# Performance work log

Hardware: AMD Instinct MI355X
Metric: run time of the kernel (lower is better)

## Reference

```python
import jax, jax.numpy as jnp
import numpy as np

B, L, D, H = 2, 4096, 512, 8
DK = D // H
SCALE = 1.0 / float(np.sqrt(DK))


def setup_inputs() -> dict:
    key = jax.random.key(0)
    k1, k2, k3 = jax.random.split(key, 3)
    x = jax.random.normal(k1, (B, L, D), dtype=jnp.float32)
    w_qkv = jax.random.normal(k2, (3 * D, D), dtype=jnp.float32) * 0.02
    w_o = jax.random.normal(k3, (D, D), dtype=jnp.float32) * 0.02
    return {"x": x, "w_qkv": w_qkv, "w_o": w_o}


def reference(x, w_qkv, w_o):
    b, l, d = x.shape
    # qkv projection: Linear(d, 3d, bias=False) -> x @ W^T
    qkv = (x @ w_qkv.T).reshape(b, l, 3, H, DK).transpose(2, 0, 3, 1, 4)  # [3,B,H,L,dk]
    q, k, v = qkv[0], qkv[1], qkv[2]
    # naive O(L^2) attention (faithful to source)
    scores = jnp.einsum("bhld,bhmd->bhlm", q, k) * SCALE  # [B,H,L,L]
    attn = jax.nn.softmax(scores, axis=-1)
    ctx = jnp.einsum("bhlm,bhmd->bhld", attn, v)  # [B,H,L,dk]
    ctx = ctx.transpose(0, 2, 1, 3).reshape(b, l, d)
    return ctx @ w_o.T
```

## Files before the change

### kernel.cpp

```cpp
#include <hip/hip_runtime.h>


#define Bq 2
#define Lq 4096
#define Dq 512
#define Hq 8
#define DKq 64
#define PST 72

using short8  = __attribute__((ext_vector_type(8))) short;
using float4v = __attribute__((ext_vector_type(4))) float;
using half4   = __attribute__((ext_vector_type(4))) _Float16;
typedef unsigned short u16;
typedef unsigned int   u32;

__device__ __forceinline__ u16 f2bf(float f) {
    u32 u = __float_as_uint(f);
    u += 0x7fffu + ((u >> 16) & 1u);
    return (u16)(u >> 16);
}

__device__ __forceinline__ float4v mfma16(short8 a, short8 b, float4v c) {
    return __builtin_amdgcn_mfma_f32_16x16x32_bf16(a, b, c, 0, 0, 0);
}

__device__ __forceinline__ void gload_lds16(const u16* g, u16* l) {
    __builtin_amdgcn_global_load_lds(
        (const __attribute__((address_space(1))) unsigned int*)g,
        (__attribute__((address_space(3))) unsigned int*)l,
        16, 0, 0);
}

__global__ __launch_bounds__(256) void castall(const float* __restrict__ x,
                                               const float* __restrict__ wq,
                                               const float* __restrict__ wo,
                                               u16* __restrict__ xb,
                                               u16* __restrict__ wqb,
                                               u16* __restrict__ wob) {
    int g = blockIdx.x;
    const float* s; u16* d; int base;
    if (g < 4096)      { s = x;  d = xb;  base = g * 1024; }
    else if (g < 4864) { s = wq; d = wqb; base = (g - 4096) * 1024; }
    else               { s = wo; d = wob; base = (g - 4864) * 1024; }
    int i = base + threadIdx.x * 4;
    float4 f = *(const float4*)&s[i];
    ushort4 o;
    o.x = f2bf(f.x); o.y = f2bf(f.y); o.z = f2bf(f.z); o.w = f2bf(f.w);
    *(ushort4*)&d[i] = o;
}

__global__ __launch_bounds__(256) void qkv_gemm(const u16* __restrict__ A,
                                                const u16* __restrict__ Bw,
                                                u16* __restrict__ qb,
                                                u16* __restrict__ kb,
                                                u16* __restrict__ vt) {
    __shared__ __align__(16) u16 As[128 * 64];
    __shared__ __align__(16) u16 Bs[128 * 64];
    const int m0 = blockIdx.x * 128, n0 = blockIdx.y * 128;
    const int tid = threadIdx.x, w = tid >> 6, lane = tid & 63;
    const int l15 = lane & 15, quad = lane >> 4;
    const int wy = w & 1, wx = w >> 1;
    const int r8 = lane >> 3, c8 = lane & 7, csw = c8 ^ r8;
    const int sw = l15 & 7;

    float4v acc[4][4];
    float4v zero = {0.f, 0.f, 0.f, 0.f};
#pragma unroll
    for (int mi = 0; mi < 4; mi++)
#pragma unroll
        for (int ni = 0; ni < 4; ni++) acc[mi][ni] = zero;

    for (int k0 = 0; k0 < 512; k0 += 64) {
#pragma unroll
        for (int i = 0; i < 4; i++) {
            int row = w * 32 + i * 8;
            gload_lds16(&A[(size_t)(m0 + row + r8) * 512 + k0 + csw * 8], &As[row * 64]);
            gload_lds16(&Bw[(size_t)(n0 + row + r8) * 512 + k0 + csw * 8], &Bs[row * 64]);
        }
        __syncthreads();
        short8 af0[4], af1[4], bf0[4], bf1[4];
#pragma unroll
        for (int t = 0; t < 4; t++) {
            int rowA = wy * 64 + t * 16 + l15;
            af0[t] = *(const short8*)&As[rowA * 64 + ((quad ^ sw) * 8)];
            af1[t] = *(const short8*)&As[rowA * 64 + (((quad + 4) ^ sw) * 8)];
            int rowB = wx * 64 + t * 16 + l15;
            bf0[t] = *(const short8*)&Bs[rowB * 64 + ((quad ^ sw) * 8)];
            bf1[t] = *(const short8*)&Bs[rowB * 64 + (((quad + 4) ^ sw) * 8)];
        }
#pragma unroll
        for (int mi = 0; mi < 4; mi++)
#pragma unroll
            for (int ni = 0; ni < 4; ni++) {
                acc[mi][ni] = mfma16(af0[mi], bf0[ni], acc[mi][ni]);
                acc[mi][ni] = mfma16(af1[mi], bf1[ni], acc[mi][ni]);
            }
        __syncthreads();
    }

#pragma unroll
    for (int mi = 0; mi < 4; mi++)
#pragma unroll
        for (int ni = 0; ni < 4; ni++) {
            int i0 = m0 + wy * 64 + mi * 16 + quad * 4;
            int j  = n0 + wx * 64 + ni * 16 + l15;
            int sel = j >> 9, rem = j & 511, h = rem >> 6, dk = rem & 63;
            int b = i0 >> 12, l = i0 & 4095;
            if (sel == 2) {
                ushort4 v4;
                v4.x = f2bf(acc[mi][ni][0]); v4.y = f2bf(acc[mi][ni][1]);
                v4.z = f2bf(acc[mi][ni][2]); v4.w = f2bf(acc[mi][ni][3]);
                *(ushort4*)&vt[((size_t)(b * Hq + h) * DKq + dk) * Lq + l] = v4;
            } else {
                u16* tgt = (sel == 0) ? qb : kb;
                float sc = (sel == 0) ? 0.125f : 1.0f;
#pragma unroll
                for (int r = 0; r < 4; r++)
                    tgt[((size_t)(b * Hq + h) * Lq + (l + r)) * DKq + dk] = f2bf(acc[mi][ni][r] * sc);
            }
        }
}

__global__ __launch_bounds__(256, 4) void attn_kern(const u16* __restrict__ qb,
                                                    const u16* __restrict__ kb,
                                                    const u16* __restrict__ vt,
                                                    _Float16* __restrict__ op0,
                                                    _Float16* __restrict__ op1,
                                                    float* __restrict__ denp) {
    __shared__ __align__(16) u16 Ks[64 * 64];
    __shared__ __align__(16) u16 Vs[64 * 64];
    __shared__ __align__(16) u16 Ps[4 * 32 * PST];
    const int g = blockIdx.x;
    const int xcd = g & 7, idx = g >> 3;
    const int bh = xcd * 2 + (idx & 1);
    const int rest = idx >> 1;
    const int split = rest & 1;
    const int q0 = (rest >> 1) * 128;
    const int tid = threadIdx.x;
    const int w = tid >> 6, lane = tid & 63, l15 = lane & 15, quad = lane >> 4;
    const int r8 = lane >> 3, c8 = lane & 7, csw = c8 ^ r8;
    const int sw = l15 & 7;

    const u16* qbase = qb + (size_t)bh * Lq * DKq;
    const u16* kbase = kb + (size_t)bh * Lq * DKq;
    const u16* vbase = vt + (size_t)bh * DKq * Lq;

    short8 aq0[2], aq1[2];
#pragma unroll
    for (int s = 0; s < 2; s++) {
        int qrow = q0 + w * 32 + s * 16 + l15;
        aq0[s] = *(const short8*)&qbase[(size_t)qrow * DKq + quad * 8];
        aq1[s] = *(const short8*)&qbase[(size_t)qrow * DKq + 32 + quad * 8];
    }

    short8 ones;
#pragma unroll
    for (int j = 0; j < 8; j++) ones[j] = (short)0x3F80;

    float4v zero = {0.f, 0.f, 0.f, 0.f};
    float4v oacc[2][4], den[2];
#pragma unroll
    for (int s = 0; s < 2; s++) {
        den[s] = zero;
#pragma unroll
        for (int n = 0; n < 4; n++) oacc[s][n] = zero;
    }

    u16* Pw = Ps + w * 32 * PST;
    const int j0base = split * 2048;

    for (int jt = 0; jt < 32; jt++) {
        int j0 = j0base + jt * 64;
        if (w < 2) {
#pragma unroll
            for (int i = 0; i < 4; i++) {
                int base = w * 32 + i * 8;
                gload_lds16(&kbase[(size_t)(j0 + base + r8) * DKq + csw * 8], &Ks[base * 64]);
            }
        } else {
#pragma unroll
            for (int i = 0; i < 4; i++) {
                int base = (w - 2) * 32 + i * 8;
                gload_lds16(&vbase[(size_t)(base + r8) * Lq + j0 + csw * 8], &Vs[base * 64]);
            }
        }
        __syncthreads();

        short8 kf0[4], kf1[4], vf0[4], vf1[4];
#pragma unroll
        for (int n = 0; n < 4; n++) {
            int row = n * 16 + l15;
            kf0[n] = *(const short8*)&Ks[row * 64 + ((quad ^ sw) * 8)];
            kf1[n] = *(const short8*)&Ks[row * 64 + (((quad + 4) ^ sw) * 8)];
            vf0[n] = *(const short8*)&Vs[row * 64 + ((quad ^ sw) * 8)];
            vf1[n] = *(const short8*)&Vs[row * 64 + (((quad + 4) ^ sw) * 8)];
        }

#pragma unroll
        for (int s = 0; s < 2; s++) {
#pragma unroll
            for (int nk = 0; nk < 4; nk++) {
                float4v sv = zero;
                sv = mfma16(kf0[nk], aq0[s], sv);
                sv = mfma16(kf1[nk], aq1[s], sv);
                u32 u0 = __float_as_uint(__expf(sv[0])) + 0x8000u;
                u32 u1 = __float_as_uint(__expf(sv[1])) + 0x8000u;
                u32 u2 = __float_as_uint(__expf(sv[2])) + 0x8000u;
                u32 u3 = __float_as_uint(__expf(sv[3])) + 0x8000u;
                uint2 pv;
                pv.x = __builtin_amdgcn_perm(u1, u0, 0x07060302u);
                pv.y = __builtin_amdgcn_perm(u3, u2, 0x07060302u);
                *(uint2*)&Pw[(s * 16 + l15) * PST + nk * 16 + quad * 4] = pv;
            }
        }

#pragma unroll
        for (int s = 0; s < 2; s++) {
            short8 ap0 = *(const short8*)&Pw[(s * 16 + l15) * PST + quad * 8];
            short8 ap1 = *(const short8*)&Pw[(s * 16 + l15) * PST + 32 + quad * 8];
            den[s] = mfma16(ap0, ones, den[s]);
            den[s] = mfma16(ap1, ones, den[s]);
#pragma unroll
            for (int n = 0; n < 4; n++) {
                oacc[s][n] = mfma16(ap0, vf0[n], oacc[s][n]);
                oacc[s][n] = mfma16(ap1, vf1[n], oacc[s][n]);
            }
        }
        __syncthreads();
    }

    _Float16* op = split ? op1 : op0;
#pragma unroll
    for (int s = 0; s < 2; s++)
#pragma unroll
        for (int r = 0; r < 4; r++) {
            float dv = den[s][r];
            float rd = __builtin_amdgcn_rcpf(dv);
            int row = q0 + w * 32 + s * 16 + quad * 4 + r;
            if (l15 == 0) denp[(size_t)(split * 16 + bh) * Lq + row] = dv;
#pragma unroll
            for (int n = 0; n < 4; n++)
                op[((size_t)bh * Lq + row) * DKq + n * 16 + l15] =
                    (_Float16)(oacc[s][n][r] * rd);
        }
}

__global__ __launch_bounds__(256) void combine(const _Float16* __restrict__ op0,
                                               const _Float16* __restrict__ op1,
                                               const float* __restrict__ denp,
                                               u16* __restrict__ ctxq) {
    int t = blockIdx.x * 256 + threadIdx.x;
    int dk4 = t & 15, l = (t >> 4) & 4095, bh = t >> 16;
    size_t r0 = (size_t)bh * Lq + l;
    half4 h0 = *(const half4*)&op0[r0 * DKq + dk4 * 4];
    half4 h1 = *(const half4*)&op1[r0 * DKq + dk4 * 4];
    float d0 = denp[r0];
    float d1 = denp[(size_t)(16 + bh) * Lq + l];
    float rs = __builtin_amdgcn_rcpf(d0 + d1);
    int b = bh >> 3, h = bh & 7;
    ushort4 o;
    o.x = f2bf(((float)h0.x * d0 + (float)h1.x * d1) * rs);
    o.y = f2bf(((float)h0.y * d0 + (float)h1.y * d1) * rs);
    o.z = f2bf(((float)h0.z * d0 + (float)h1.z * d1) * rs);
    o.w = f2bf(((float)h0.w * d0 + (float)h1.w * d1) * rs);
    *(ushort4*)&ctxq[((size_t)(b * Lq + l)) * Dq + h * DKq + dk4 * 4] = o;
}

__global__ __launch_bounds__(256) void out_gemm(const u16* __restrict__ A,
                                                const u16* __restrict__ Bw,
                                                float* __restrict__ out) {
    __shared__ __align__(16) u16 As[128 * 64];
    __shared__ __align__(16) u16 Bs[128 * 64];
    const int m0 = blockIdx.x * 128, n0 = blockIdx.y * 128;
    const int tid = threadIdx.x, w = tid >> 6, lane = tid & 63;
    const int l15 = lane & 15, quad = lane >> 4;
    const int wy = w & 1, wx = w >> 1;
    const int r8 = lane >> 3, c8 = lane & 7, csw = c8 ^ r8;
    const int sw = l15 & 7;

    float4v acc[4][4];
    float4v zero = {0.f, 0.f, 0.f, 0.f};
#pragma unroll
    for (int mi = 0; mi < 4; mi++)
#pragma unroll
        for (int ni = 0; ni < 4; ni++) acc[mi][ni] = zero;

    for (int k0 = 0; k0 < 512; k0 += 64) {
#pragma unroll
        for (int i = 0; i < 4; i++) {
            int row = w * 32 + i * 8;
            gload_lds16(&A[(size_t)(m0 + row + r8) * 512 + k0 + csw * 8], &As[row * 64]);
            gload_lds16(&Bw[(size_t)(n0 + row + r8) * 512 + k0 + csw * 8], &Bs[row * 64]);
        }
        __syncthreads();
        short8 af0[4], af1[4], bf0[4], bf1[4];
#pragma unroll
        for (int t = 0; t < 4; t++) {
            int rowA = wy * 64 + t * 16 + l15;
            af0[t] = *(const short8*)&As[rowA * 64 + ((quad ^ sw) * 8)];
            af1[t] = *(const short8*)&As[rowA * 64 + (((quad + 4) ^ sw) * 8)];
            int rowB = wx * 64 + t * 16 + l15;
            bf0[t] = *(const short8*)&Bs[rowB * 64 + ((quad ^ sw) * 8)];
            bf1[t] = *(const short8*)&Bs[rowB * 64 + (((quad + 4) ^ sw) * 8)];
        }
#pragma unroll
        for (int mi = 0; mi < 4; mi++)
#pragma unroll
            for (int ni = 0; ni < 4; ni++) {
                acc[mi][ni] = mfma16(af0[mi], bf0[ni], acc[mi][ni]);
                acc[mi][ni] = mfma16(af1[mi], bf1[ni], acc[mi][ni]);
            }
        __syncthreads();
    }

#pragma unroll
    for (int mi = 0; mi < 4; mi++)
#pragma unroll
        for (int ni = 0; ni < 4; ni++)
#pragma unroll
            for (int r = 0; r < 4; r++) {
                int i = m0 + wy * 64 + mi * 16 + quad * 4 + r;
                int j = n0 + wx * 64 + ni * 16 + l15;
                out[(size_t)i * 512 + j] = acc[mi][ni][r];
            }
}

extern "C" void kernel_launch(void* const* d_in, const int* in_sizes, int n_in,
                              void* d_out, int out_size, void* d_ws, size_t ws_size,
                              hipStream_t stream) {
    const float* x     = (const float*)d_in[0];
    const float* w_qkv = (const float*)d_in[1];
    const float* w_o   = (const float*)d_in[2];
    float* out = (float*)d_out;

    const size_t N_X   = (size_t)Bq * Lq * Dq;
    const size_t N_WQ  = (size_t)3 * Dq * Dq;
    const size_t N_WO  = (size_t)Dq * Dq;
    const size_t N_QKV = (size_t)Bq * Hq * Lq * DKq;

    u16* xb  = (u16*)d_ws;
    u16* wqb = xb + N_X;
    u16* wob = wqb + N_WQ;
    u16* qb  = wob + N_WO;
    u16* kb  = qb + N_QKV;
    u16* vt  = kb + N_QKV;
    u16* o1r = vt + N_QKV;

    _Float16* op0  = (_Float16*)xb;
    _Float16* op1  = (_Float16*)o1r;
    float*    denp = (float*)wqb;
    u16*      ctxq = qb;

    castall<<<dim3(5120), 256, 0, stream>>>(x, w_qkv, w_o, xb, wqb, wob);
    qkv_gemm<<<dim3(64, 12), 256, 0, stream>>>(xb, wqb, qb, kb, vt);
    attn_kern<<<dim3(1024), 256, 0, stream>>>(qb, kb, vt, op0, op1, denp);
    combine<<<dim3(4096), 256, 0, stream>>>(op0, op1, denp, ctxq);
    out_gemm<<<dim3(64, 4), 256, 0, stream>>>(ctxq, wob, out);
}
```

Baseline: 198.9 us.

## Rework attention tiling with double-buffered K/V and LDS-staged GEMM epilogues

The attention kernel now gives each wave a 64-query by 32-key quadrant instead of 32 queries by all 64 keys. It keeps P in registers and feeds it straight into 16x16x16 bf16 MFMAs, which removes the LDS round trip for P. K/V tiles are double-buffered so the next tile loads while the current one is computed, and partial sums from the two key-halves are reduced through LDS at the end. Separately, the QKV and output GEMM epilogues stage results in padded LDS so global stores are wide and coalesced (including the V transpose). The costs are more registers per wave (the occupancy hint was dropped), extra synchronisation for the cross-wave reduction, and use of the smaller MFMA shape.

```diff
diff --git a/kernel.cpp b/kernel.cpp
--- a/kernel.cpp
+++ b/kernel.cpp
@@ -6,9 +6,10 @@
 #define Dq 512
 #define Hq 8
 #define DKq 64
-#define PST 72
 
 using short8  = __attribute__((ext_vector_type(8))) short;
+using short4v = __attribute__((ext_vector_type(4))) short;
+using ushort8 = __attribute__((ext_vector_type(8))) unsigned short;
 using float4v = __attribute__((ext_vector_type(4))) float;
 using half4   = __attribute__((ext_vector_type(4))) _Float16;
 typedef unsigned short u16;
@@ -22,6 +23,17 @@
 
 __device__ __forceinline__ float4v mfma16(short8 a, short8 b, float4v c) {
     return __builtin_amdgcn_mfma_f32_16x16x32_bf16(a, b, c, 0, 0, 0);
+}
+
+__device__ __forceinline__ float4v mfma1k(short4v a, short4v b, float4v c) {
+#if __has_builtin(__builtin_amdgcn_mfma_f32_16x16x16bf16_1k)
+    return __builtin_amdgcn_mfma_f32_16x16x16bf16_1k(a, b, c, 0, 0, 0);
+#else
+    float4v d;
+    asm volatile("v_mfma_f32_16x16x16_bf16 %0, %1, %2, %3"
+                 : "=v"(d) : "v"(a), "v"(b), "v"(c));
+    return d;
+#endif
 }
 
 __device__ __forceinline__ void gload_lds16(const u16* g, u16* l) {
@@ -54,8 +66,10 @@
                                                 u16* __restrict__ qb,
                                                 u16* __restrict__ kb,
                                                 u16* __restrict__ vt) {
-    __shared__ __align__(16) u16 As[128 * 64];
-    __shared__ __align__(16) u16 Bs[128 * 64];
+    __shared__ __align__(16) union {
+        struct { u16 A[128 * 64]; u16 B[128 * 64]; } s;
+        u16 epi[128 * 134];
+    } sm;
     const int m0 = blockIdx.x * 128, n0 = blockIdx.y * 128;
     const int tid = threadIdx.x, w = tid >> 6, lane = tid & 63;
     const int l15 = lane & 15, quad = lane >> 4;
@@ -74,19 +88,19 @@
 #pragma unroll
         for (int i = 0; i < 4; i++) {
             int row = w * 32 + i * 8;
-            gload_lds16(&A[(size_t)(m0 + row + r8) * 512 + k0 + csw * 8], &As[row * 64]);
-            gload_lds16(&Bw[(size_t)(n0 + row + r8) * 512 + k0 + csw * 8], &Bs[row * 64]);
+            gload_lds16(&A[(size_t)(m0 + row + r8) * 512 + k0 + csw * 8], &sm.s.A[row * 64]);
+            gload_lds16(&Bw[(size_t)(n0 + row + r8) * 512 + k0 + csw * 8], &sm.s.B[row * 64]);
         }
         __syncthreads();
         short8 af0[4], af1[4], bf0[4], bf1[4];
 #pragma unroll
         for (int t = 0; t < 4; t++) {
             int rowA = wy * 64 + t * 16 + l15;
-            af0[t] = *(const short8*)&As[rowA * 64 + ((quad ^ sw) * 8)];
-            af1[t] = *(const short8*)&As[rowA * 64 + (((quad + 4) ^ sw) * 8)];
+            af0[t] = *(const short8*)&sm.s.A[rowA * 64 + ((quad ^ sw) * 8)];
+            af1[t] = *(const short8*)&sm.s.A[rowA * 64 + (((quad + 4) ^ sw) * 8)];
             int rowB = wx * 64 + t * 16 + l15;
-            bf0[t] = *(const short8*)&Bs[rowB * 64 + ((quad ^ sw) * 8)];
-            bf1[t] = *(const short8*)&Bs[rowB * 64 + (((quad + 4) ^ sw) * 8)];
+            bf0[t] = *(const short8*)&sm.s.B[rowB * 64 + ((quad ^ sw) * 8)];
+            bf1[t] = *(const short8*)&sm.s.B[rowB * 64 + (((quad + 4) ^ sw) * 8)];
         }
 #pragma unroll
         for (int mi = 0; mi < 4; mi++)
@@ -98,46 +112,66 @@
         __syncthreads();
     }
 
-#pragma unroll
-    for (int mi = 0; mi < 4; mi++)
-#pragma unroll
-        for (int ni = 0; ni < 4; ni++) {
-            int i0 = m0 + wy * 64 + mi * 16 + quad * 4;
-            int j  = n0 + wx * 64 + ni * 16 + l15;
-            int sel = j >> 9, rem = j & 511, h = rem >> 6, dk = rem & 63;
-            int b = i0 >> 12, l = i0 & 4095;
-            if (sel == 2) {
+    const int sel = n0 >> 9;
+    if (sel < 2) {
+        const float sc = (sel == 0) ? 0.125f : 1.0f;
+#pragma unroll
+        for (int mi = 0; mi < 4; mi++)
+#pragma unroll
+            for (int ni = 0; ni < 4; ni++)
+#pragma unroll
+                for (int r = 0; r < 4; r++)
+                    sm.epi[(wy * 64 + mi * 16 + quad * 4 + r) * 134 + wx * 64 + ni * 16 + l15] =
+                        f2bf(acc[mi][ni][r] * sc);
+        __syncthreads();
+        u16* tgt = (sel == 0) ? qb : kb;
+#pragma unroll
+        for (int i = 0; i < 8; i++) {
+            int flat = i * 2048 + tid * 8;
+            int row = flat >> 7, col = flat & 127;
+            ushort8 vv = *(const ushort8*)&sm.epi[row * 134 + col];
+            int dg = (n0 & 511) + col, h = dg >> 6, dk = dg & 63;
+            int mm = m0 + row, b = mm >> 12, l = mm & 4095;
+            *(ushort8*)&tgt[((size_t)(b * Hq + h) * Lq + l) * DKq + dk] = vv;
+        }
+    } else {
+#pragma unroll
+        for (int mi = 0; mi < 4; mi++)
+#pragma unroll
+            for (int ni = 0; ni < 4; ni++) {
                 ushort4 v4;
                 v4.x = f2bf(acc[mi][ni][0]); v4.y = f2bf(acc[mi][ni][1]);
                 v4.z = f2bf(acc[mi][ni][2]); v4.w = f2bf(acc[mi][ni][3]);
-                *(ushort4*)&vt[((size_t)(b * Hq + h) * DKq + dk) * Lq + l] = v4;
-            } else {
-                u16* tgt = (sel == 0) ? qb : kb;
-                float sc = (sel == 0) ? 0.125f : 1.0f;
-#pragma unroll
-                for (int r = 0; r < 4; r++)
-                    tgt[((size_t)(b * Hq + h) * Lq + (l + r)) * DKq + dk] = f2bf(acc[mi][ni][r] * sc);
-            }
-        }
-}
-
-__global__ __launch_bounds__(256, 4) void attn_kern(const u16* __restrict__ qb,
-                                                    const u16* __restrict__ kb,
-                                                    const u16* __restrict__ vt,
-                                                    _Float16* __restrict__ op0,
-                                                    _Float16* __restrict__ op1,
-                                                    float* __restrict__ denp) {
-    __shared__ __align__(16) u16 Ks[64 * 64];
-    __shared__ __align__(16) u16 Vs[64 * 64];
-    __shared__ __align__(16) u16 Ps[4 * 32 * PST];
+                *(ushort4*)&sm.epi[(wx * 64 + ni * 16 + l15) * 134 + wy * 64 + mi * 16 + quad * 4] = v4;
+            }
+        __syncthreads();
+#pragma unroll
+        for (int i = 0; i < 8; i++) {
+            int flat = i * 2048 + tid * 8;
+            int vrow = flat >> 7, vcol = flat & 127;
+            ushort8 vv = *(const ushort8*)&sm.epi[vrow * 134 + vcol];
+            int dg = (n0 & 511) + vrow, h = dg >> 6, dk = dg & 63;
+            int mm = m0 + vcol, b = mm >> 12, l = mm & 4095;
+            *(ushort8*)&vt[((size_t)(b * Hq + h) * DKq + dk) * Lq + l] = vv;
+        }
+    }
+}
+
+__global__ __launch_bounds__(256) void attn_kern(const u16* __restrict__ qb,
+                                                 const u16* __restrict__ kb,
+                                                 const u16* __restrict__ vt,
+                                                 _Float16* __restrict__ op0,
+                                                 _Float16* __restrict__ op1,
+                                                 float* __restrict__ denp) {
+    __shared__ __align__(16) u16 KV[2][2][64 * 64];
     const int g = blockIdx.x;
-    const int xcd = g & 7, idx = g >> 3;
-    const int bh = xcd * 2 + (idx & 1);
-    const int rest = idx >> 1;
+    const int bh = (g & 7) * 2 + ((g >> 3) & 1);
+    const int rest = g >> 4;
     const int split = rest & 1;
     const int q0 = (rest >> 1) * 128;
     const int tid = threadIdx.x;
     const int w = tid >> 6, lane = tid & 63, l15 = lane & 15, quad = lane >> 4;
+    const int wq = w & 1, wk = w >> 1;
     const int r8 = lane >> 3, c8 = lane & 7, csw = c8 ^ r8;
     const int sw = l15 & 7;
 
@@ -145,104 +179,146 @@
     const u16* kbase = kb + (size_t)bh * Lq * DKq;
     const u16* vbase = vt + (size_t)bh * DKq * Lq;
 
-    short8 aq0[2], aq1[2];
-#pragma unroll
-    for (int s = 0; s < 2; s++) {
-        int qrow = q0 + w * 32 + s * 16 + l15;
+    short8 aq0[4], aq1[4];
+#pragma unroll
+    for (int s = 0; s < 4; s++) {
+        int qrow = q0 + wq * 64 + s * 16 + l15;
         aq0[s] = *(const short8*)&qbase[(size_t)qrow * DKq + quad * 8];
         aq1[s] = *(const short8*)&qbase[(size_t)qrow * DKq + 32 + quad * 8];
     }
 
-    short8 ones;
-#pragma unroll
-    for (int j = 0; j < 8; j++) ones[j] = (short)0x3F80;
-
+    short4v ones4 = {(short)0x3F80, (short)0x3F80, (short)0x3F80, (short)0x3F80};
     float4v zero = {0.f, 0.f, 0.f, 0.f};
-    float4v oacc[2][4], den[2];
-#pragma unroll
-    for (int s = 0; s < 2; s++) {
+    float4v oacc[4][4], den[4];
+#pragma unroll
+    for (int s = 0; s < 4; s++) {
         den[s] = zero;
 #pragma unroll
         for (int n = 0; n < 4; n++) oacc[s][n] = zero;
     }
 
-    u16* Pw = Ps + w * 32 * PST;
     const int j0base = split * 2048;
-
-    for (int jt = 0; jt < 32; jt++) {
-        int j0 = j0base + jt * 64;
+    {
+        int j0 = j0base;
         if (w < 2) {
 #pragma unroll
             for (int i = 0; i < 4; i++) {
                 int base = w * 32 + i * 8;
-                gload_lds16(&kbase[(size_t)(j0 + base + r8) * DKq + csw * 8], &Ks[base * 64]);
+                gload_lds16(&kbase[(size_t)(j0 + base + r8) * DKq + csw * 8], &KV[0][0][base * 64]);
             }
         } else {
 #pragma unroll
             for (int i = 0; i < 4; i++) {
                 int base = (w - 2) * 32 + i * 8;
-                gload_lds16(&vbase[(size_t)(base + r8) * Lq + j0 + csw * 8], &Vs[base * 64]);
-            }
-        }
-        __syncthreads();
-
-        short8 kf0[4], kf1[4], vf0[4], vf1[4];
-#pragma unroll
-        for (int n = 0; n < 4; n++) {
-            int row = n * 16 + l15;
-            kf0[n] = *(const short8*)&Ks[row * 64 + ((quad ^ sw) * 8)];
-            kf1[n] = *(const short8*)&Ks[row * 64 + (((quad + 4) ^ sw) * 8)];
-            vf0[n] = *(const short8*)&Vs[row * 64 + ((quad ^ sw) * 8)];
-            vf1[n] = *(const short8*)&Vs[row * 64 + (((quad + 4) ^ sw) * 8)];
-        }
-
-#pragma unroll
-        for (int s = 0; s < 2; s++) {
-#pragma unroll
-            for (int nk = 0; nk < 4; nk++) {
-                float4v sv = zero;
-                sv = mfma16(kf0[nk], aq0[s], sv);
-                sv = mfma16(kf1[nk], aq1[s], sv);
+                gload_lds16(&vbase[(size_t)(base + r8) * Lq + j0 + csw * 8], &KV[0][1][base * 64]);
+            }
+        }
+    }
+
+    int p = 0;
+    for (int jt = 0; jt < 32; jt++) {
+        __syncthreads();
+        if (jt < 31) {
+            int j0 = j0base + (jt + 1) * 64;
+            if (w < 2) {
+#pragma unroll
+                for (int i = 0; i < 4; i++) {
+                    int base = w * 32 + i * 8;
+                    gload_lds16(&kbase[(size_t)(j0 + base + r8) * DKq + csw * 8], &KV[p ^ 1][0][base * 64]);
+                }
+            } else {
+#pragma unroll
+                for (int i = 0; i < 4; i++) {
+                    int base = (w - 2) * 32 + i * 8;
+                    gload_lds16(&vbase[(size_t)(base + r8) * Lq + j0 + csw * 8], &KV[p ^ 1][1][base * 64]);
+                }
+            }
+        }
+        const u16* Kb = KV[p][0];
+        const u16* Vb = KV[p][1];
+#pragma unroll
+        for (int nkk = 0; nkk < 2; nkk++) {
+            int krow = wk * 32 + nkk * 16 + l15;
+            short8 k0 = *(const short8*)&Kb[krow * 64 + ((quad ^ sw) * 8)];
+            short8 k1 = *(const short8*)&Kb[krow * 64 + (((quad + 4) ^ sw) * 8)];
+            int kc = ((wk * 4 + nkk * 2 + (quad >> 1)) ^ sw) * 8 + (quad & 1) * 4;
+            short4v vf[4];
+#pragma unroll
+            for (int n = 0; n < 4; n++)
+                vf[n] = *(const short4v*)&Vb[(n * 16 + l15) * 64 + kc];
+#pragma unroll
+            for (int s = 0; s < 4; s++) {
+                float4v sv = mfma16(k0, aq0[s], zero);
+                sv = mfma16(k1, aq1[s], sv);
                 u32 u0 = __float_as_uint(__expf(sv[0])) + 0x8000u;
                 u32 u1 = __float_as_uint(__expf(sv[1])) + 0x8000u;
                 u32 u2 = __float_as_uint(__expf(sv[2])) + 0x8000u;
                 u32 u3 = __float_as_uint(__expf(sv[3])) + 0x8000u;
-                uint2 pv;
-                pv.x = __builtin_amdgcn_perm(u1, u0, 0x07060302u);
-                pv.y = __builtin_amdgcn_perm(u3, u2, 0x07060302u);
-                *(uint2*)&Pw[(s * 16 + l15) * PST + nk * 16 + quad * 4] = pv;
-            }
-        }
-
-#pragma unroll
-        for (int s = 0; s < 2; s++) {
-            short8 ap0 = *(const short8*)&Pw[(s * 16 + l15) * PST + quad * 8];
-            short8 ap1 = *(const short8*)&Pw[(s * 16 + l15) * PST + 32 + quad * 8];
-            den[s] = mfma16(ap0, ones, den[s]);
-            den[s] = mfma16(ap1, ones, den[s]);
-#pragma unroll
-            for (int n = 0; n < 4; n++) {
-                oacc[s][n] = mfma16(ap0, vf0[n], oacc[s][n]);
-                oacc[s][n] = mfma16(ap1, vf1[n], oacc[s][n]);
-            }
-        }
-        __syncthreads();
-    }
-
-    _Float16* op = split ? op1 : op0;
-#pragma unroll
-    for (int s = 0; s < 2; s++)
-#pragma unroll
-        for (int r = 0; r < 4; r++) {
-            float dv = den[s][r];
-            float rd = __builtin_amdgcn_rcpf(dv);
-            int row = q0 + w * 32 + s * 16 + quad * 4 + r;
-            if (l15 == 0) denp[(size_t)(split * 16 + bh) * Lq + row] = dv;
-#pragma unroll
-            for (int n = 0; n < 4; n++)
-                op[((size_t)bh * Lq + row) * DKq + n * 16 + l15] =
-                    (_Float16)(oacc[s][n][r] * rd);
-        }
+                union { uint2 u; short4v s4; } cv;
+                cv.u.x = __builtin_amdgcn_perm(u1, u0, 0x07060302u);
+                cv.u.y = __builtin_amdgcn_perm(u3, u2, 0x07060302u);
+                short4v pf = cv.s4;
+                den[s] = mfma1k(pf, ones4, den[s]);
+#pragma unroll
+                for (int n = 0; n < 4; n++)
+                    oacc[s][n] = mfma1k(pf, vf[n], oacc[s][n]);
+            }
+        }
+        p ^= 1;
+    }
+    __syncthreads();
+
+    float4v* sc4 = (float4v*)&KV[0][0][0];
+    if (wk == 1) {
+        float4v* dst = sc4 + (size_t)(wq * 64 + lane) * 13;
+#pragma unroll
+        for (int s = 0; s < 4; s++) dst[s] = den[s];
+#pragma unroll
+        for (int s = 0; s < 2; s++)
+#pragma unroll
+            for (int n = 0; n < 4; n++) dst[4 + s * 4 + n] = oacc[s][n];
+    }
+    __syncthreads();
+    if (wk == 0) {
+        float4v* src = sc4 + (size_t)(wq * 64 + lane) * 13;
+#pragma unroll
+        for (int s = 0; s < 4; s++) den[s] += src[s];
+#pragma unroll
+        for (int s = 0; s < 2; s++)
+#pragma unroll
+            for (int n = 0; n < 4; n++) oacc[s][n] += src[4 + s * 4 + n];
+    }
+    __syncthreads();
+    if (wk == 1) {
+        float4v* dst = sc4 + (size_t)(wq * 64 + lane) * 9;
+#pragma unroll
+        for (int s = 2; s < 4; s++)
+#pragma unroll
+            for (int n = 0; n < 4; n++) dst[(s - 2) * 4 + n] = oacc[s][n];
+    }
+    __syncthreads();
+    if (wk == 0) {
+        float4v* src = sc4 + (size_t)(wq * 64 + lane) * 9;
+#pragma unroll
+        for (int s = 2; s < 4; s++)
+#pragma unroll
+            for (int n = 0; n < 4; n++) oacc[s][n] += src[(s - 2) * 4 + n];
+
+        _Float16* op = split ? op1 : op0;
+#pragma unroll
+        for (int s = 0; s < 4; s++)
+#pragma unroll
+            for (int r = 0; r < 4; r++) {
+                float dv = den[s][r];
+                float rd = __builtin_amdgcn_rcpf(dv);
+                int row = q0 + wq * 64 + s * 16 + quad * 4 + r;
+                if (l15 == 0) denp[(size_t)(split * 16 + bh) * Lq + row] = dv;
+#pragma unroll
+                for (int n = 0; n < 4; n++)
+                    op[((size_t)bh * Lq + row) * DKq + n * 16 + l15] =
+                        (_Float16)(oacc[s][n][r] * rd);
+            }
+    }
 }
 
 __global__ __launch_bounds__(256) void combine(const _Float16* __restrict__ op0,
@@ -269,8 +345,10 @@
 __global__ __launch_bounds__(256) void out_gemm(const u16* __restrict__ A,
                                                 const u16* __restrict__ Bw,
                                                 float* __restrict__ out) {
-    __shared__ __align__(16) u16 As[128 * 64];
-    __shared__ __align__(16) u16 Bs[128 * 64];
+    __shared__ __align__(16) union {
+        struct { u16 A[128 * 64]; u16 B[128 * 64]; } s;
+        float fepi[64 * 132];
+    } sm;
     const int m0 = blockIdx.x * 128, n0 = blockIdx.y * 128;
     const int tid = threadIdx.x, w = tid >> 6, lane = tid & 63;
     const int l15 = lane & 15, quad = lane >> 4;
@@ -289,19 +367,19 @@
 #pragma unroll
         for (int i = 0; i < 4; i++) {
             int row = w * 32 + i * 8;
-            gload_lds16(&A[(size_t)(m0 + row + r8) * 512 + k0 + csw * 8], &As[row * 64]);
-            gload_lds16(&Bw[(size_t)(n0 + row + r8) * 512 + k0 + csw * 8], &Bs[row * 64]);
+            gload_lds16(&A[(size_t)(m0 + row + r8) * 512 + k0 + csw * 8], &sm.s.A[row * 64]);
+            gload_lds16(&Bw[(size_t)(n0 + row + r8) * 512 + k0 + csw * 8], &sm.s.B[row * 64]);
         }
         __syncthreads();
         short8 af0[4], af1[4], bf0[4], bf1[4];
 #pragma unroll
         for (int t = 0; t < 4; t++) {
             int rowA = wy * 64 + t * 16 + l15;
-            af0[t] = *(const short8*)&As[rowA * 64 + ((quad ^ sw) * 8)];
-            af1[t] = *(const short8*)&As[rowA * 64 + (((quad + 4) ^ sw) * 8)];
+            af0[t] = *(const short8*)&sm.s.A[rowA * 64 + ((quad ^ sw) * 8)];
+            af1[t] = *(const short8*)&sm.s.A[rowA * 64 + (((quad + 4) ^ sw) * 8)];
             int rowB = wx * 64 + t * 16 + l15;
-            bf0[t] = *(const short8*)&Bs[rowB * 64 + ((quad ^ sw) * 8)];
-            bf1[t] = *(const short8*)&Bs[rowB * 64 + (((quad + 4) ^ sw) * 8)];
+            bf0[t] = *(const short8*)&sm.s.B[rowB * 64 + ((quad ^ sw) * 8)];
+            bf1[t] = *(const short8*)&sm.s.B[rowB * 64 + (((quad + 4) ^ sw) * 8)];
         }
 #pragma unroll
         for (int mi = 0; mi < 4; mi++)
@@ -314,15 +392,28 @@
     }
 
 #pragma unroll
-    for (int mi = 0; mi < 4; mi++)
-#pragma unroll
-        for (int ni = 0; ni < 4; ni++)
-#pragma unroll
-            for (int r = 0; r < 4; r++) {
-                int i = m0 + wy * 64 + mi * 16 + quad * 4 + r;
-                int j = n0 + wx * 64 + ni * 16 + l15;
-                out[(size_t)i * 512 + j] = acc[mi][ni][r];
-            }
+    for (int ph = 0; ph < 2; ph++) {
+#pragma unroll
+        for (int mh = 0; mh < 2; mh++) {
+            int mi = ph * 2 + mh;
+            int lr = wy * 32 + mh * 16 + quad * 4;
+#pragma unroll
+            for (int ni = 0; ni < 4; ni++)
+#pragma unroll
+                for (int r = 0; r < 4; r++)
+                    sm.fepi[(lr + r) * 132 + wx * 64 + ni * 16 + l15] = acc[mi][ni][r];
+        }
+        __syncthreads();
+#pragma unroll
+        for (int i = 0; i < 8; i++) {
+            int flat = i * 1024 + tid * 4;
+            int lrow = flat >> 7, col = flat & 127;
+            float4 vv = *(const float4*)&sm.fepi[lrow * 132 + col];
+            int m = (lrow & 31) + (lrow >> 5) * 64 + ph * 32;
+            *(float4*)&out[(size_t)(m0 + m) * 512 + n0 + col] = vv;
+        }
+        __syncthreads();
+    }
 }
 
 extern "C" void kernel_launch(void* const* d_in, const int* in_sizes, int n_in,
```

Measured after the change: 207.3 us. +4.2%, slower.

## Fuse split-combine into output GEMM and stage GEMM epilogues through LDS

Applied to the files above, without the earlier changes.

Drops the separate combine kernel. The output GEMM now reads the two fp16 partial attention outputs and their denominators, normalises them, and writes bf16 tiles straight into shared memory. The QKV and output GEMM epilogues now stage results in LDS and write coalesced 16-byte vectors instead of scattered scalar stores. The attention P buffer swaps row padding for an XOR swizzle. This removes one launch and an intermediate round trip through memory. In exchange the output GEMM repeats the combine math for each of its 4 column blocks and loses the async load path for A.

```diff
diff --git a/kernel.cpp b/kernel.cpp
--- a/kernel.cpp
+++ b/kernel.cpp
@@ -6,11 +6,10 @@
 #define Dq 512
 #define Hq 8
 #define DKq 64
-#define PST 72
 
 using short8  = __attribute__((ext_vector_type(8))) short;
+using ushort8 = __attribute__((ext_vector_type(8))) unsigned short;
 using float4v = __attribute__((ext_vector_type(4))) float;
-using half4   = __attribute__((ext_vector_type(4))) _Float16;
 typedef unsigned short u16;
 typedef unsigned int   u32;
 
@@ -54,8 +53,10 @@
                                                 u16* __restrict__ qb,
                                                 u16* __restrict__ kb,
                                                 u16* __restrict__ vt) {
-    __shared__ __align__(16) u16 As[128 * 64];
-    __shared__ __align__(16) u16 Bs[128 * 64];
+    __shared__ __align__(16) union {
+        struct { u16 A[128 * 64]; u16 B[128 * 64]; } s;
+        u16 epi[128 * 134];
+    } sm;
     const int m0 = blockIdx.x * 128, n0 = blockIdx.y * 128;
     const int tid = threadIdx.x, w = tid >> 6, lane = tid & 63;
     const int l15 = lane & 15, quad = lane >> 4;
@@ -74,19 +75,19 @@
 #pragma unroll
         for (int i = 0; i < 4; i++) {
             int row = w * 32 + i * 8;
-            gload_lds16(&A[(size_t)(m0 + row + r8) * 512 + k0 + csw * 8], &As[row * 64]);
-            gload_lds16(&Bw[(size_t)(n0 + row + r8) * 512 + k0 + csw * 8], &Bs[row * 64]);
+            gload_lds16(&A[(size_t)(m0 + row + r8) * 512 + k0 + csw * 8], &sm.s.A[row * 64]);
+            gload_lds16(&Bw[(size_t)(n0 + row + r8) * 512 + k0 + csw * 8], &sm.s.B[row * 64]);
         }
         __syncthreads();
         short8 af0[4], af1[4], bf0[4], bf1[4];
 #pragma unroll
         for (int t = 0; t < 4; t++) {
             int rowA = wy * 64 + t * 16 + l15;
-            af0[t] = *(const short8*)&As[rowA * 64 + ((quad ^ sw) * 8)];
-            af1[t] = *(const short8*)&As[rowA * 64 + (((quad + 4) ^ sw) * 8)];
+            af0[t] = *(const short8*)&sm.s.A[rowA * 64 + ((quad ^ sw) * 8)];
+            af1[t] = *(const short8*)&sm.s.A[rowA * 64 + (((quad + 4) ^ sw) * 8)];
             int rowB = wx * 64 + t * 16 + l15;
-            bf0[t] = *(const short8*)&Bs[rowB * 64 + ((quad ^ sw) * 8)];
-            bf1[t] = *(const short8*)&Bs[rowB * 64 + (((quad + 4) ^ sw) * 8)];
+            bf0[t] = *(const short8*)&sm.s.B[rowB * 64 + ((quad ^ sw) * 8)];
+            bf1[t] = *(const short8*)&sm.s.B[rowB * 64 + (((quad + 4) ^ sw) * 8)];
         }
 #pragma unroll
         for (int mi = 0; mi < 4; mi++)
@@ -98,27 +99,49 @@
         __syncthreads();
     }
 
-#pragma unroll
-    for (int mi = 0; mi < 4; mi++)
-#pragma unroll
-        for (int ni = 0; ni < 4; ni++) {
-            int i0 = m0 + wy * 64 + mi * 16 + quad * 4;
-            int j  = n0 + wx * 64 + ni * 16 + l15;
-            int sel = j >> 9, rem = j & 511, h = rem >> 6, dk = rem & 63;
-            int b = i0 >> 12, l = i0 & 4095;
-            if (sel == 2) {
+    const int sel = n0 >> 9;
+    if (sel < 2) {
+        const float sc = (sel == 0) ? 0.125f : 1.0f;
+#pragma unroll
+        for (int mi = 0; mi < 4; mi++)
+#pragma unroll
+            for (int ni = 0; ni < 4; ni++)
+#pragma unroll
+                for (int r = 0; r < 4; r++)
+                    sm.epi[(wy * 64 + mi * 16 + quad * 4 + r) * 134 + wx * 64 + ni * 16 + l15] =
+                        f2bf(acc[mi][ni][r] * sc);
+        __syncthreads();
+        u16* tgt = (sel == 0) ? qb : kb;
+#pragma unroll
+        for (int i = 0; i < 8; i++) {
+            int flat = i * 2048 + tid * 8;
+            int row = flat >> 7, col = flat & 127;
+            ushort8 vv = *(const ushort8*)&sm.epi[row * 134 + col];
+            int dg = (n0 & 511) + col, h = dg >> 6, dk = dg & 63;
+            int mm = m0 + row, b = mm >> 12, l = mm & 4095;
+            *(ushort8*)&tgt[((size_t)(b * Hq + h) * Lq + l) * DKq + dk] = vv;
+        }
+    } else {
+#pragma unroll
+        for (int mi = 0; mi < 4; mi++)
+#pragma unroll
+            for (int ni = 0; ni < 4; ni++) {
                 ushort4 v4;
                 v4.x = f2bf(acc[mi][ni][0]); v4.y = f2bf(acc[mi][ni][1]);
                 v4.z = f2bf(acc[mi][ni][2]); v4.w = f2bf(acc[mi][ni][3]);
-                *(ushort4*)&vt[((size_t)(b * Hq + h) * DKq + dk) * Lq + l] = v4;
-            } else {
-                u16* tgt = (sel == 0) ? qb : kb;
-                float sc = (sel == 0) ? 0.125f : 1.0f;
-#pragma unroll
-                for (int r = 0; r < 4; r++)
-                    tgt[((size_t)(b * Hq + h) * Lq + (l + r)) * DKq + dk] = f2bf(acc[mi][ni][r] * sc);
-            }
-        }
+                *(ushort4*)&sm.epi[(wx * 64 + ni * 16 + l15) * 134 + wy * 64 + mi * 16 + quad * 4] = v4;
+            }
+        __syncthreads();
+#pragma unroll
+        for (int i = 0; i < 8; i++) {
+            int flat = i * 2048 + tid * 8;
+            int vrow = flat >> 7, vcol = flat & 127;
+            ushort8 vv = *(const ushort8*)&sm.epi[vrow * 134 + vcol];
+            int dg = (n0 & 511) + vrow, h = dg >> 6, dk = dg & 63;
+            int mm = m0 + vcol, b = mm >> 12, l = mm & 4095;
+            *(ushort8*)&vt[((size_t)(b * Hq + h) * DKq + dk) * Lq + l] = vv;
+        }
+    }
 }
 
 __global__ __launch_bounds__(256, 4) void attn_kern(const u16* __restrict__ qb,
@@ -129,11 +152,10 @@
                                                     float* __restrict__ denp) {
     __shared__ __align__(16) u16 Ks[64 * 64];
     __shared__ __align__(16) u16 Vs[64 * 64];
-    __shared__ __align__(16) u16 Ps[4 * 32 * PST];
+    __shared__ __align__(16) u16 Ps[4 * 32 * 64];
     const int g = blockIdx.x;
-    const int xcd = g & 7, idx = g >> 3;
-    const int bh = xcd * 2 + (idx & 1);
-    const int rest = idx >> 1;
+    const int bh = (g & 7) * 2 + ((g >> 3) & 1);
+    const int rest = g >> 4;
     const int split = rest & 1;
     const int q0 = (rest >> 1) * 128;
     const int tid = threadIdx.x;
@@ -153,9 +175,9 @@
         aq1[s] = *(const short8*)&qbase[(size_t)qrow * DKq + 32 + quad * 8];
     }
 
-    short8 ones;
-#pragma unroll
-    for (int j = 0; j < 8; j++) ones[j] = (short)0x3F80;
+    short8 ones8;
+#pragma unroll
+    for (int j = 0; j < 8; j++) ones8[j] = (short)0x3F80;
 
     float4v zero = {0.f, 0.f, 0.f, 0.f};
     float4v oacc[2][4], den[2];
@@ -166,7 +188,7 @@
         for (int n = 0; n < 4; n++) oacc[s][n] = zero;
     }
 
-    u16* Pw = Ps + w * 32 * PST;
+    u16* Pw = Ps + w * 32 * 64;
     const int j0base = split * 2048;
 
     for (int jt = 0; jt < 32; jt++) {
@@ -210,16 +232,17 @@
                 uint2 pv;
                 pv.x = __builtin_amdgcn_perm(u1, u0, 0x07060302u);
                 pv.y = __builtin_amdgcn_perm(u3, u2, 0x07060302u);
-                *(uint2*)&Pw[(s * 16 + l15) * PST + nk * 16 + quad * 4] = pv;
+                int chunk = (nk * 2 + (quad >> 1)) ^ sw;
+                *(uint2*)&Pw[(s * 16 + l15) * 64 + chunk * 8 + (quad & 1) * 4] = pv;
             }
         }
 
 #pragma unroll
         for (int s = 0; s < 2; s++) {
-            short8 ap0 = *(const short8*)&Pw[(s * 16 + l15) * PST + quad * 8];
-            short8 ap1 = *(const short8*)&Pw[(s * 16 + l15) * PST + 32 + quad * 8];
-            den[s] = mfma16(ap0, ones, den[s]);
-            den[s] = mfma16(ap1, ones, den[s]);
+            short8 ap0 = *(const short8*)&Pw[(s * 16 + l15) * 64 + ((quad ^ sw) * 8)];
+            short8 ap1 = *(const short8*)&Pw[(s * 16 + l15) * 64 + (((quad + 4) ^ sw) * 8)];
+            den[s] = mfma16(ap0, ones8, den[s]);
+            den[s] = mfma16(ap1, ones8, den[s]);
 #pragma unroll
             for (int n = 0; n < 4; n++) {
                 oacc[s][n] = mfma16(ap0, vf0[n], oacc[s][n]);
@@ -245,32 +268,15 @@
         }
 }
 
-__global__ __launch_bounds__(256) void combine(const _Float16* __restrict__ op0,
-                                               const _Float16* __restrict__ op1,
-                                               const float* __restrict__ denp,
-                                               u16* __restrict__ ctxq) {
-    int t = blockIdx.x * 256 + threadIdx.x;
-    int dk4 = t & 15, l = (t >> 4) & 4095, bh = t >> 16;
-    size_t r0 = (size_t)bh * Lq + l;
-    half4 h0 = *(const half4*)&op0[r0 * DKq + dk4 * 4];
-    half4 h1 = *(const half4*)&op1[r0 * DKq + dk4 * 4];
-    float d0 = denp[r0];
-    float d1 = denp[(size_t)(16 + bh) * Lq + l];
-    float rs = __builtin_amdgcn_rcpf(d0 + d1);
-    int b = bh >> 3, h = bh & 7;
-    ushort4 o;
-    o.x = f2bf(((float)h0.x * d0 + (float)h1.x * d1) * rs);
-    o.y = f2bf(((float)h0.y * d0 + (float)h1.y * d1) * rs);
-    o.z = f2bf(((float)h0.z * d0 + (float)h1.z * d1) * rs);
-    o.w = f2bf(((float)h0.w * d0 + (float)h1.w * d1) * rs);
-    *(ushort4*)&ctxq[((size_t)(b * Lq + l)) * Dq + h * DKq + dk4 * 4] = o;
-}
-
-__global__ __launch_bounds__(256) void out_gemm(const u16* __restrict__ A,
+__global__ __launch_bounds__(256) void out_gemm(const _Float16* __restrict__ op0,
+                                                const _Float16* __restrict__ op1,
+                                                const float* __restrict__ denp,
                                                 const u16* __restrict__ Bw,
                                                 float* __restrict__ out) {
-    __shared__ __align__(16) u16 As[128 * 64];
-    __shared__ __align__(16) u16 Bs[128 * 64];
+    __shared__ __align__(16) union {
+        struct { u16 A[128 * 64]; u16 B[128 * 64]; } s;
+        float fepi[64 * 132];
+    } sm;
     const int m0 = blockIdx.x * 128, n0 = blockIdx.y * 128;
     const int tid = threadIdx.x, w = tid >> 6, lane = tid & 63;
     const int l15 = lane & 15, quad = lane >> 4;
@@ -286,22 +292,37 @@
         for (int ni = 0; ni < 4; ni++) acc[mi][ni] = zero;
 
     for (int k0 = 0; k0 < 512; k0 += 64) {
+        const int kk = k0 >> 6;
 #pragma unroll
         for (int i = 0; i < 4; i++) {
             int row = w * 32 + i * 8;
-            gload_lds16(&A[(size_t)(m0 + row + r8) * 512 + k0 + csw * 8], &As[row * 64]);
-            gload_lds16(&Bw[(size_t)(n0 + row + r8) * 512 + k0 + csw * 8], &Bs[row * 64]);
+            gload_lds16(&Bw[(size_t)(n0 + row + r8) * 512 + k0 + csw * 8], &sm.s.B[row * 64]);
+            int mm = m0 + row + r8;
+            int b = mm >> 12, l = mm & 4095;
+            int bh = b * Hq + kk;
+            size_t rowoff = ((size_t)bh * Lq + l) * DKq + csw * 8;
+            union { float4 f; _Float16 h[8]; } ua, ub;
+            ua.f = *(const float4*)&op0[rowoff];
+            ub.f = *(const float4*)&op1[rowoff];
+            float d0 = denp[(size_t)bh * Lq + l];
+            float d1 = denp[(size_t)(16 + bh) * Lq + l];
+            float rs = __builtin_amdgcn_rcpf(d0 + d1);
+            ushort8 ov;
+#pragma unroll
+            for (int j = 0; j < 8; j++)
+                ov[j] = f2bf(((float)ua.h[j] * d0 + (float)ub.h[j] * d1) * rs);
+            *(ushort8*)&sm.s.A[(row + r8) * 64 + c8 * 8] = ov;
         }
         __syncthreads();
         short8 af0[4], af1[4], bf0[4], bf1[4];
 #pragma unroll
         for (int t = 0; t < 4; t++) {
             int rowA = wy * 64 + t * 16 + l15;
-            af0[t] = *(const short8*)&As[rowA * 64 + ((quad ^ sw) * 8)];
-            af1[t] = *(const short8*)&As[rowA * 64 + (((quad + 4) ^ sw) * 8)];
+            af0[t] = *(const short8*)&sm.s.A[rowA * 64 + ((quad ^ sw) * 8)];
+            af1[t] = *(const short8*)&sm.s.A[rowA * 64 + (((quad + 4) ^ sw) * 8)];
             int rowB = wx * 64 + t * 16 + l15;
-            bf0[t] = *(const short8*)&Bs[rowB * 64 + ((quad ^ sw) * 8)];
-            bf1[t] = *(const short8*)&Bs[rowB * 64 + (((quad + 4) ^ sw) * 8)];
+            bf0[t] = *(const short8*)&sm.s.B[rowB * 64 + ((quad ^ sw) * 8)];
+            bf1[t] = *(const short8*)&sm.s.B[rowB * 64 + (((quad + 4) ^ sw) * 8)];
         }
 #pragma unroll
         for (int mi = 0; mi < 4; mi++)
@@ -314,15 +335,28 @@
     }
 
 #pragma unroll
-    for (int mi = 0; mi < 4; mi++)
-#pragma unroll
-        for (int ni = 0; ni < 4; ni++)
-#pragma unroll
-            for (int r = 0; r < 4; r++) {
-                int i = m0 + wy * 64 + mi * 16 + quad * 4 + r;
-                int j = n0 + wx * 64 + ni * 16 + l15;
-                out[(size_t)i * 512 + j] = acc[mi][ni][r];
-            }
+    for (int ph = 0; ph < 2; ph++) {
+#pragma unroll
+        for (int mh = 0; mh < 2; mh++) {
+            int mi = ph * 2 + mh;
+            int lr = wy * 32 + mh * 16 + quad * 4;
+#pragma unroll
+            for (int ni = 0; ni < 4; ni++)
+#pragma unroll
+                for (int r = 0; r < 4; r++)
+                    sm.fepi[(lr + r) * 132 + wx * 64 + ni * 16 + l15] = acc[mi][ni][r];
+        }
+        __syncthreads();
+#pragma unroll
+        for (int i = 0; i < 8; i++) {
+            int flat = i * 1024 + tid * 4;
+            int lrow = flat >> 7, col = flat & 127;
+            float4 vv = *(const float4*)&sm.fepi[lrow * 132 + col];
+            int m = (lrow & 31) + (lrow >> 5) * 64 + ph * 32;
+            *(float4*)&out[(size_t)(m0 + m) * 512 + n0 + col] = vv;
+        }
+        __syncthreads();
+    }
 }
 
 extern "C" void kernel_launch(void* const* d_in, const int* in_sizes, int n_in,
@@ -349,11 +383,9 @@
     _Float16* op0  = (_Float16*)xb;
     _Float16* op1  = (_Float16*)o1r;
     float*    denp = (float*)wqb;
-    u16*      ctxq = qb;
 
     castall<<<dim3(5120), 256, 0, stream>>>(x, w_qkv, w_o, xb, wqb, wob);
     qkv_gemm<<<dim3(64, 12), 256, 0, stream>>>(xb, wqb, qb, kb, vt);
     attn_kern<<<dim3(1024), 256, 0, stream>>>(qb, kb, vt, op0, op1, denp);
-    combine<<<dim3(4096), 256, 0, stream>>>(op0, op1, denp, ctxq);
-    out_gemm<<<dim3(64, 4), 256, 0, stream>>>(ctxq, wob, out);
-}
+    out_gemm<<<dim3(64, 4), 256, 0, stream>>>(op0, op1, denp, wob, out);
+}
```

Measured after the change: 349.7 us. +75.8%, slower.
